# Kernel tuning notes

Measured on AMD Instinct MI355X. Metric: run time of the kernel, lower is better.

The kernel has to match this reference:

```python
import jax, jax.numpy as jnp
import numpy as np

W_KERNEL = 5      # dilation kernel size (w)
K_BG = 0.1        # background weight (k)
RELAX = 5.0       # sigmoid temperature (relax)
INF = 1e4         # 'no zero in column' sentinel (>> image diagonal)
EPS = 1e-7        # DiceLoss eps


def setup_inputs() -> dict:
    key = jax.random.key(0)
    k1, k2 = jax.random.split(key)
    B, H, W = 32, 256, 256
    preds = jax.random.normal(k1, (B, H, W), dtype=jnp.float32)
    targets = (jax.random.uniform(k2, (B, H, W)) > 0.99).astype(jnp.float32)
    return {"preds": preds, "targets": targets}


def _dilate(t, w):
    # cv2.dilate with w x w ones kernel == sliding-window max, SAME padding
    pad = w // 2
    return jax.lax.reduce_window(t, -jnp.inf, jax.lax.max,
                                 (1, w, w), (1, 1, 1),
                                 [(0, 0), (pad, pad), (pad, pad)])


def _vertical_dist(zero_mask):
    # per-column distance (in rows) to nearest zero pixel; [B,H,W] -> [B,H,W]
    B, H, W = zero_mask.shape
    rows = jnp.moveaxis(zero_mask, 1, 0)  # [H,B,W]

    def step(carry, z):
        d = jnp.where(z, 0.0, jnp.minimum(carry + 1.0, INF))
        return d, d

    init = jnp.full((B, W), INF, dtype=jnp.float32)
    _, fwd = jax.lax.scan(step, init, rows)
    _, bwd = jax.lax.scan(step, init, rows[::-1])
    g = jnp.minimum(fwd, bwd[::-1])  # [H,B,W]
    return jnp.moveaxis(g, 0, 1)


def _edt(fat):
    # exact euclidean distance transform (distance to nearest zero pixel),
    # separable two-pass: vertical 1D distance, then horizontal min-plus.
    B, H, W = fat.shape
    g = _vertical_dist(fat == 0)  # [B,H,W]
    col = jnp.arange(W, dtype=jnp.float32)
    off2 = (col[:, None] - col[None, :]) ** 2  # [W_j, W_k]

    def per_img(gi):  # gi: [H,W]
        # d2[i,j] = min_k g[i,k]^2 + (j-k)^2   -> [H,W,W] intermediate
        d2 = jnp.min(gi[:, None, :] ** 2 + off2[None, :, :], axis=-1)
        return jnp.sqrt(d2)

    return jax.lax.map(per_img, g)  # sequential over batch caps memory


def _distance_maps(targets):
    fat = _dilate(targets, W_KERNEL)          # [B,H,W]
    d = _edt(fat)                              # [B,H,W]
    soft = jax.nn.sigmoid(d / RELAX)
    soft = soft - jnp.min(soft, axis=(1, 2), keepdims=True)
    mx = jnp.max(soft, axis=(1, 2), keepdims=True)
    soft = soft / jnp.where(mx > 0, mx, 1.0)
    dm_soft = soft + (1.0 - fat) * K_BG
    has_fg = jnp.max(targets, axis=(1, 2), keepdims=True) > 0
    return jnp.where(has_fg, dm_soft, 1.0 - targets)


def reference(preds, targets):
    p = jax.nn.sigmoid(preds)
    dm = jax.lax.stop_gradient(_distance_maps(targets))  # computed in numpy in torch => constant
    pw = p * dm
    bs = pw.shape[0]
    y_pred = pw.reshape(bs, 1, -1)
    y_true = targets.reshape(bs, 1, -1)
    # smp DiceLoss('binary', from_logits=False): dims=(0,2), smooth=0, eps=1e-7
    inter = jnp.sum(y_pred * y_true, axis=(0, 2))
    card = jnp.sum(y_pred + y_true, axis=(0, 2))
    dice = (2.0 * inter) / jnp.maximum(card, EPS)
    loss = 1.0 - dice
    mask = (jnp.sum(y_true, axis=(0, 2)) > 0).astype(loss.dtype)
    return jnp.mean(loss * mask)
```

## Files before the change

### kernel.cpp

```cpp
#include <hip/hip_runtime.h>
#include <math.h>

#define BB 32
#define HH 256
#define WW 256
#define HW (HH*WW)
#define TOT (BB*HW)
#define K_BG 0.1f
#define RELAX 5.0f
#define EPS_D 1e-7

typedef unsigned long long u64;
typedef unsigned short u16;

__device__ __forceinline__ float sigf(float x) { return 1.0f / (1.0f + expf(-x)); }

__global__ void k_maskdil(const float* __restrict__ tg, u64* __restrict__ dmask) {
    __shared__ u64 nz[20][4];
    __shared__ u64 hd[20][4];
    int blk = blockIdx.x;
    int b = blk >> 4, band = blk & 15;
    int r0 = band * 16;
    int t = threadIdx.x, w = t >> 6;
    const float* img = tg + b * HW;
    for (int rr = 0; rr < 20; ++rr) {
        int rg = r0 + rr - 2;
        float v = (rg >= 0 && rg < HH) ? img[rg * WW + t] : 0.0f;
        u64 bal = __ballot(v != 0.0f);
        if ((t & 63) == 0) nz[rr][w] = bal;
    }
    __syncthreads();
    if (t < 80) {
        int rr = t >> 2, k = t & 3;
        u64 m = nz[rr][k];
        u64 ml = (k > 0) ? nz[rr][k - 1] : 0ULL;
        u64 mr = (k < 3) ? nz[rr][k + 1] : 0ULL;
        hd[rr][k] = m | (m << 1) | (m << 2) | (m >> 1) | (m >> 2)
                  | (ml >> 62) | (ml >> 63) | (mr << 62) | (mr << 63);
    }
    __syncthreads();
    if (t < 64) {
        int rr = t >> 2, k = t & 3;
        u64 o = hd[rr][k] | hd[rr + 1][k] | hd[rr + 2][k] | hd[rr + 3][k] | hd[rr + 4][k];
        dmask[b * 1024 + (r0 + rr) * 4 + k] = o;
    }
}

__global__ __launch_bounds__(256) void k_mega(const float* __restrict__ preds,
                                              const float* __restrict__ tg,
                                              const u64* __restrict__ dmask,
                                              float4* __restrict__ part1,
                                              float4* __restrict__ part2) {
    __shared__ u64 mk[1024];
    __shared__ u16 gS[WW];
    __shared__ float red[8][4];
    int row = blockIdx.x;
    int b = row >> 8, i = row & 255;
    int t = threadIdx.x;

    float p  = preds[row * WW + t];
    float tv = tg[row * WW + t];

    const uint4* src4 = (const uint4*)(dmask + b * 1024);
    uint4* mk4 = (uint4*)mk;
    mk4[t] = src4[t];
    mk4[t + 256] = src4[t + 256];
    __syncthreads();

    int j = t, w = j >> 6;
    u64 bitm = 1ULL << (j & 63);
    int fgbit = (mk[i * 4 + w] & bitm) ? 1 : 0;
    int g0 = 0;
    if (fgbit) {
        int up = 10000;
        for (int k = 1; k <= i; ++k)
            if (!(mk[(i - k) * 4 + w] & bitm)) { up = k; break; }
        int dn = 10000;
        for (int k = 1; k < HH - i; ++k)
            if (!(mk[(i + k) * 4 + w] & bitm)) { dn = k; break; }
        g0 = min(up, dn);
    }
    gS[j] = (u16)g0;
    __syncthreads();

    float gv = (float)g0;
    float best = gv * gv;
    for (int r = 1; r < WW; ++r) {
        float rr = (float)(r * r);
        if (rr >= best) break;
        int jl = j - r, jr = j + r;
        if (jl >= 0) { float v = (float)gS[jl]; best = fminf(best, v * v + rr); }
        if (jr < WW) { float v = (float)gS[jr]; best = fminf(best, v * v + rr); }
    }
    float dv = sqrtf(best);

    float sp = sigf(p);
    float sd = sigf(dv / RELAX);
    float vals[8];
    vals[0] = sp * sd * tv;
    vals[1] = sp * tv;
    vals[2] = sp * sd;
    vals[3] = sp;
    vals[4] = sp * (1.0f - (float)fgbit);
    vals[5] = tv;
    vals[6] = dv;
    vals[7] = dv;
    for (int off = 32; off > 0; off >>= 1) {
        #pragma unroll
        for (int q = 0; q < 6; ++q) vals[q] += __shfl_down(vals[q], off, 64);
        vals[6] = fminf(vals[6], __shfl_down(vals[6], off, 64));
        vals[7] = fmaxf(vals[7], __shfl_down(vals[7], off, 64));
    }
    int wid = t >> 6, lane = t & 63;
    if (lane == 0) {
        #pragma unroll
        for (int q = 0; q < 8; ++q) red[q][wid] = vals[q];
    }
    __syncthreads();
    if (t == 0) {
        float s[8];
        #pragma unroll
        for (int q = 0; q < 6; ++q) s[q] = red[q][0] + red[q][1] + red[q][2] + red[q][3];
        s[6] = fminf(fminf(red[6][0], red[6][1]), fminf(red[6][2], red[6][3]));
        s[7] = fmaxf(fmaxf(red[7][0], red[7][1]), fmaxf(red[7][2], red[7][3]));
        part1[row] = make_float4(s[0], s[1], s[2], s[3]);
        part2[row] = make_float4(s[4], s[5], s[6], s[7]);
    }
}

__global__ void k_img(const float4* __restrict__ part1, const float4* __restrict__ part2,
                      float4* __restrict__ imgout) {
    __shared__ float red[8][4];
    int b = blockIdx.x, t = threadIdx.x;
    float4 p1 = part1[b * HH + t];
    float4 p2 = part2[b * HH + t];
    float vals[8] = {p1.x, p1.y, p1.z, p1.w, p2.x, p2.y, p2.z, p2.w};
    for (int off = 32; off > 0; off >>= 1) {
        #pragma unroll
        for (int q = 0; q < 6; ++q) vals[q] += __shfl_down(vals[q], off, 64);
        vals[6] = fminf(vals[6], __shfl_down(vals[6], off, 64));
        vals[7] = fmaxf(vals[7], __shfl_down(vals[7], off, 64));
    }
    int wid = t >> 6, lane = t & 63;
    if (lane == 0) {
        #pragma unroll
        for (int q = 0; q < 8; ++q) red[q][wid] = vals[q];
    }
    __syncthreads();
    if (t == 0) {
        float A  = red[0][0] + red[0][1] + red[0][2] + red[0][3];
        float Bs = red[1][0] + red[1][1] + red[1][2] + red[1][3];
        float Ap = red[2][0] + red[2][1] + red[2][2] + red[2][3];
        float Bp = red[3][0] + red[3][1] + red[3][2] + red[3][3];
        float Cp = red[4][0] + red[4][1] + red[4][2] + red[4][3];
        float T  = red[5][0] + red[5][1] + red[5][2] + red[5][3];
        float dmn = fminf(fminf(red[6][0], red[6][1]), fminf(red[6][2], red[6][3]));
        float dmx = fmaxf(fmaxf(red[7][0], red[7][1]), fmaxf(red[7][2], red[7][3]));
        float inter, card, any;
        if (dmx > 0.0f) {
            float smin = sigf(dmn / RELAX);
            float smax = sigf(dmx / RELAX);
            float m = smax - smin;
            float denom = (m > 0.0f) ? m : 1.0f;
            inter = (A - smin * Bs) / denom;
            card  = (Ap - smin * Bp) / denom + K_BG * Cp + T;
            any = 1.0f;
        } else {
            inter = 0.0f;
            card = Bp - Bs + T;
            any = 0.0f;
        }
        imgout[b] = make_float4(inter, card, any, 0.0f);
    }
}

__global__ void k_fin(const float4* __restrict__ imgout, float* __restrict__ out) {
    if (threadIdx.x == 0) {
        double I = 0.0, C = 0.0;
        int any = 0;
        for (int b = 0; b < BB; ++b) {
            float4 v = imgout[b];
            I += (double)v.x; C += (double)v.y;
            any |= (v.z > 0.0f);
        }
        double dice = 2.0 * I / fmax(C, (double)EPS_D);
        out[0] = any ? (float)(1.0 - dice) : 0.0f;
    }
}

extern "C" void kernel_launch(void* const* d_in, const int* in_sizes, int n_in,
                              void* d_out, int out_size, void* d_ws, size_t ws_size,
                              hipStream_t stream) {
    const float* preds = (const float*)d_in[0];
    const float* tg    = (const float*)d_in[1];
    float* out = (float*)d_out;

    u64* dmask   = (u64*)d_ws;
    float4* part1 = (float4*)(dmask + BB * 1024);
    float4* part2 = part1 + BB * HH;
    float4* imgout = part2 + BB * HH;

    hipLaunchKernelGGL(k_maskdil, dim3(BB * 16), dim3(WW), 0, stream, tg, dmask);
    hipLaunchKernelGGL(k_mega, dim3(BB * HH), dim3(WW), 0, stream, preds, tg, dmask,
                       part1, part2);
    hipLaunchKernelGGL(k_img, dim3(BB), dim3(HH), 0, stream, part1, part2, imgout);
    hipLaunchKernelGGL(k_fin, dim3(1), dim3(64), 0, stream, imgout, out);
}
```

Before: 103.1 us.

## Fuse per-image and final reductions into main kernel via last-block atomics

Removes the separate per-image reduction and final dice kernels. The last block to finish each image, detected with an atomic counter, does that image's reduction, and the last image block computes the scalar loss. It also stops rereading the float targets in the main kernel: the target value is rebuilt from a bitmask written by the mask kernel. This saves two kernel launches and the 8 MB target reread, at the cost of thread fences and atomics, and relies on the counters being reset by the first kernel on every call.

```diff
diff --git a/kernel.cpp b/kernel.cpp
--- a/kernel.cpp
+++ b/kernel.cpp
@@ -15,13 +15,15 @@
 
 __device__ __forceinline__ float sigf(float x) { return 1.0f / (1.0f + expf(-x)); }
 
-__global__ void k_maskdil(const float* __restrict__ tg, u64* __restrict__ dmask) {
+__global__ void k_maskdil(const float* __restrict__ tg, u64* __restrict__ dmask,
+                          u64* __restrict__ nzmask, int* __restrict__ cnt) {
     __shared__ u64 nz[20][4];
     __shared__ u64 hd[20][4];
     int blk = blockIdx.x;
     int b = blk >> 4, band = blk & 15;
     int r0 = band * 16;
     int t = threadIdx.x, w = t >> 6;
+    if (blk == 0 && t < 33) cnt[t] = 0;
     const float* img = tg + b * HW;
     for (int rr = 0; rr < 20; ++rr) {
         int rg = r0 + rr - 2;
@@ -38,6 +40,10 @@
         hd[rr][k] = m | (m << 1) | (m << 2) | (m >> 1) | (m >> 2)
                   | (ml >> 62) | (ml >> 63) | (mr << 62) | (mr << 63);
     }
+    if (t < 64) {
+        int rr = t >> 2, k = t & 3;
+        nzmask[b * 1024 + (r0 + rr) * 4 + k] = nz[rr + 2][k];
+    }
     __syncthreads();
     if (t < 64) {
         int rr = t >> 2, k = t & 3;
@@ -47,19 +53,22 @@
 }
 
 __global__ __launch_bounds__(256) void k_mega(const float* __restrict__ preds,
-                                              const float* __restrict__ tg,
                                               const u64* __restrict__ dmask,
+                                              const u64* __restrict__ nzmask,
                                               float4* __restrict__ part1,
-                                              float4* __restrict__ part2) {
+                                              float4* __restrict__ part2,
+                                              float4* __restrict__ imgout,
+                                              int* __restrict__ cnt,
+                                              float* __restrict__ out) {
     __shared__ u64 mk[1024];
     __shared__ u16 gS[WW];
     __shared__ float red[8][4];
+    __shared__ int lastA;
     int row = blockIdx.x;
     int b = row >> 8, i = row & 255;
     int t = threadIdx.x;
 
-    float p  = preds[row * WW + t];
-    float tv = tg[row * WW + t];
+    float p = preds[row * WW + t];
 
     const uint4* src4 = (const uint4*)(dmask + b * 1024);
     uint4* mk4 = (uint4*)mk;
@@ -69,6 +78,7 @@
 
     int j = t, w = j >> 6;
     u64 bitm = 1ULL << (j & 63);
+    float tv = (float)((nzmask[b * 1024 + i * 4 + w] >> (j & 63)) & 1ULL);
     int fgbit = (mk[i * 4 + w] & bitm) ? 1 : 0;
     int g0 = 0;
     if (fgbit) {
@@ -125,66 +135,67 @@
         s[7] = fmaxf(fmaxf(red[7][0], red[7][1]), fmaxf(red[7][2], red[7][3]));
         part1[row] = make_float4(s[0], s[1], s[2], s[3]);
         part2[row] = make_float4(s[4], s[5], s[6], s[7]);
-    }
-}
-
-__global__ void k_img(const float4* __restrict__ part1, const float4* __restrict__ part2,
-                      float4* __restrict__ imgout) {
-    __shared__ float red[8][4];
-    int b = blockIdx.x, t = threadIdx.x;
-    float4 p1 = part1[b * HH + t];
-    float4 p2 = part2[b * HH + t];
-    float vals[8] = {p1.x, p1.y, p1.z, p1.w, p2.x, p2.y, p2.z, p2.w};
-    for (int off = 32; off > 0; off >>= 1) {
-        #pragma unroll
-        for (int q = 0; q < 6; ++q) vals[q] += __shfl_down(vals[q], off, 64);
-        vals[6] = fminf(vals[6], __shfl_down(vals[6], off, 64));
-        vals[7] = fmaxf(vals[7], __shfl_down(vals[7], off, 64));
-    }
-    int wid = t >> 6, lane = t & 63;
-    if (lane == 0) {
-        #pragma unroll
-        for (int q = 0; q < 8; ++q) red[q][wid] = vals[q];
-    }
-    __syncthreads();
-    if (t == 0) {
-        float A  = red[0][0] + red[0][1] + red[0][2] + red[0][3];
-        float Bs = red[1][0] + red[1][1] + red[1][2] + red[1][3];
-        float Ap = red[2][0] + red[2][1] + red[2][2] + red[2][3];
-        float Bp = red[3][0] + red[3][1] + red[3][2] + red[3][3];
-        float Cp = red[4][0] + red[4][1] + red[4][2] + red[4][3];
-        float T  = red[5][0] + red[5][1] + red[5][2] + red[5][3];
-        float dmn = fminf(fminf(red[6][0], red[6][1]), fminf(red[6][2], red[6][3]));
-        float dmx = fmaxf(fmaxf(red[7][0], red[7][1]), fmaxf(red[7][2], red[7][3]));
-        float inter, card, any;
-        if (dmx > 0.0f) {
-            float smin = sigf(dmn / RELAX);
-            float smax = sigf(dmx / RELAX);
-            float m = smax - smin;
-            float denom = (m > 0.0f) ? m : 1.0f;
-            inter = (A - smin * Bs) / denom;
-            card  = (Ap - smin * Bp) / denom + K_BG * Cp + T;
-            any = 1.0f;
-        } else {
-            inter = 0.0f;
-            card = Bp - Bs + T;
-            any = 0.0f;
-        }
-        imgout[b] = make_float4(inter, card, any, 0.0f);
-    }
-}
-
-__global__ void k_fin(const float4* __restrict__ imgout, float* __restrict__ out) {
-    if (threadIdx.x == 0) {
-        double I = 0.0, C = 0.0;
-        int any = 0;
-        for (int b = 0; b < BB; ++b) {
-            float4 v = imgout[b];
-            I += (double)v.x; C += (double)v.y;
-            any |= (v.z > 0.0f);
-        }
-        double dice = 2.0 * I / fmax(C, (double)EPS_D);
-        out[0] = any ? (float)(1.0 - dice) : 0.0f;
+        __threadfence();
+        int old = atomicAdd(&cnt[b], 1);
+        lastA = (old == 255);
+    }
+    __syncthreads();
+
+    if (lastA) {
+        float4 p1 = part1[b * HH + t];
+        float4 p2 = part2[b * HH + t];
+        float v2[8] = {p1.x, p1.y, p1.z, p1.w, p2.x, p2.y, p2.z, p2.w};
+        for (int off = 32; off > 0; off >>= 1) {
+            #pragma unroll
+            for (int q = 0; q < 6; ++q) v2[q] += __shfl_down(v2[q], off, 64);
+            v2[6] = fminf(v2[6], __shfl_down(v2[6], off, 64));
+            v2[7] = fmaxf(v2[7], __shfl_down(v2[7], off, 64));
+        }
+        if (lane == 0) {
+            #pragma unroll
+            for (int q = 0; q < 8; ++q) red[q][wid] = v2[q];
+        }
+        __syncthreads();
+        int lastB = 0;
+        if (t == 0) {
+            float A  = red[0][0] + red[0][1] + red[0][2] + red[0][3];
+            float Bs = red[1][0] + red[1][1] + red[1][2] + red[1][3];
+            float Ap = red[2][0] + red[2][1] + red[2][2] + red[2][3];
+            float Bp = red[3][0] + red[3][1] + red[3][2] + red[3][3];
+            float Cp = red[4][0] + red[4][1] + red[4][2] + red[4][3];
+            float T  = red[5][0] + red[5][1] + red[5][2] + red[5][3];
+            float dmn = fminf(fminf(red[6][0], red[6][1]), fminf(red[6][2], red[6][3]));
+            float dmx = fmaxf(fmaxf(red[7][0], red[7][1]), fmaxf(red[7][2], red[7][3]));
+            float inter, card, any;
+            if (dmx > 0.0f) {
+                float smin = sigf(dmn / RELAX);
+                float smax = sigf(dmx / RELAX);
+                float m = smax - smin;
+                float denom = (m > 0.0f) ? m : 1.0f;
+                inter = (A - smin * Bs) / denom;
+                card  = (Ap - smin * Bp) / denom + K_BG * Cp + T;
+                any = 1.0f;
+            } else {
+                inter = 0.0f;
+                card = Bp - Bs + T;
+                any = 0.0f;
+            }
+            imgout[b] = make_float4(inter, card, any, 0.0f);
+            __threadfence();
+            int old2 = atomicAdd(&cnt[32], 1);
+            lastB = (old2 == BB - 1);
+        }
+        if (t == 0 && lastB) {
+            double I = 0.0, C = 0.0;
+            int any = 0;
+            for (int bb = 0; bb < BB; ++bb) {
+                float4 v = imgout[bb];
+                I += (double)v.x; C += (double)v.y;
+                any |= (v.z > 0.0f);
+            }
+            double dice = 2.0 * I / fmax(C, (double)EPS_D);
+            out[0] = any ? (float)(1.0 - dice) : 0.0f;
+        }
     }
 }
 
@@ -195,14 +206,14 @@
     const float* tg    = (const float*)d_in[1];
     float* out = (float*)d_out;
 
-    u64* dmask   = (u64*)d_ws;
-    float4* part1 = (float4*)(dmask + BB * 1024);
+    u64* dmask    = (u64*)d_ws;
+    u64* nzmask   = dmask + BB * 1024;
+    float4* part1 = (float4*)(nzmask + BB * 1024);
     float4* part2 = part1 + BB * HH;
     float4* imgout = part2 + BB * HH;
-
-    hipLaunchKernelGGL(k_maskdil, dim3(BB * 16), dim3(WW), 0, stream, tg, dmask);
-    hipLaunchKernelGGL(k_mega, dim3(BB * HH), dim3(WW), 0, stream, preds, tg, dmask,
-                       part1, part2);
-    hipLaunchKernelGGL(k_img, dim3(BB), dim3(HH), 0, stream, part1, part2, imgout);
-    hipLaunchKernelGGL(k_fin, dim3(1), dim3(64), 0, stream, imgout, out);
+    int* cnt = (int*)(imgout + BB);
+
+    hipLaunchKernelGGL(k_maskdil, dim3(BB * 16), dim3(WW), 0, stream, tg, dmask, nzmask, cnt);
+    hipLaunchKernelGGL(k_mega, dim3(BB * HH), dim3(WW), 0, stream, preds, dmask, nzmask,
+                       part1, part2, imgout, cnt, out);
 }
```

New measurement: 247.0 us. 2.4x slower.

## Use bit-transposed column masks and clz/ffs scans for vertical distances, 4 rows per block

Applied to the files above, without the earlier changes.

The dilated mask is now stored column-major per 64-bit word and bit-transposed in registers with shuffle butterflies, so each thread holds its column as four 64-bit words. The nearest zero above and below is then found with clz/ffs instead of a serial per-row loop. Each block handles 4 rows, which amortises the mask transpose and cuts the block count and partial sums. The target values are read from a packed nonzero bitmask rather than the float tensor. This adds transpose and shuffle work per block and raises per-thread register use.

```diff
diff --git a/kernel.cpp b/kernel.cpp
--- a/kernel.cpp
+++ b/kernel.cpp
@@ -5,7 +5,6 @@
 #define HH 256
 #define WW 256
 #define HW (HH*WW)
-#define TOT (BB*HW)
 #define K_BG 0.1f
 #define RELAX 5.0f
 #define EPS_D 1e-7
@@ -15,7 +14,12 @@
 
 __device__ __forceinline__ float sigf(float x) { return 1.0f / (1.0f + expf(-x)); }
 
-__global__ void k_maskdil(const float* __restrict__ tg, u64* __restrict__ dmask) {
+__device__ __forceinline__ u64 shflx64(u64 x, int s) {
+    return (u64)__shfl_xor((unsigned long long)x, s, 64);
+}
+
+__global__ void k_maskdil(const float* __restrict__ tg, u64* __restrict__ dmaskT,
+                          u64* __restrict__ nzmask) {
     __shared__ u64 nz[20][4];
     __shared__ u64 hd[20][4];
     int blk = blockIdx.x;
@@ -38,124 +42,159 @@
         hd[rr][k] = m | (m << 1) | (m << 2) | (m >> 1) | (m >> 2)
                   | (ml >> 62) | (ml >> 63) | (mr << 62) | (mr << 63);
     }
+    if (t < 64) {
+        int rr = t >> 2, k = t & 3;
+        nzmask[b * 1024 + (r0 + rr) * 4 + k] = nz[rr + 2][k];
+    }
     __syncthreads();
     if (t < 64) {
         int rr = t >> 2, k = t & 3;
         u64 o = hd[rr][k] | hd[rr + 1][k] | hd[rr + 2][k] | hd[rr + 3][k] | hd[rr + 4][k];
-        dmask[b * 1024 + (r0 + rr) * 4 + k] = o;
+        dmaskT[b * 1024 + k * 256 + (r0 + rr)] = o;
     }
 }
 
 __global__ __launch_bounds__(256) void k_mega(const float* __restrict__ preds,
-                                              const float* __restrict__ tg,
-                                              const u64* __restrict__ dmask,
+                                              const u64* __restrict__ dmaskT,
+                                              const u64* __restrict__ nzmask,
                                               float4* __restrict__ part1,
                                               float4* __restrict__ part2) {
-    __shared__ u64 mk[1024];
-    __shared__ u16 gS[WW];
+    __shared__ u64 colT[4 * 256];
+    __shared__ u16 gS[4][WW];
     __shared__ float red[8][4];
-    int row = blockIdx.x;
-    int b = row >> 8, i = row & 255;
-    int t = threadIdx.x;
-
-    float p  = preds[row * WW + t];
-    float tv = tg[row * WW + t];
-
-    const uint4* src4 = (const uint4*)(dmask + b * 1024);
-    uint4* mk4 = (uint4*)mk;
-    mk4[t] = src4[t];
-    mk4[t + 256] = src4[t + 256];
-    __syncthreads();
-
-    int j = t, w = j >> 6;
-    u64 bitm = 1ULL << (j & 63);
-    int fgbit = (mk[i * 4 + w] & bitm) ? 1 : 0;
-    int g0 = 0;
-    if (fgbit) {
-        int up = 10000;
-        for (int k = 1; k <= i; ++k)
-            if (!(mk[(i - k) * 4 + w] & bitm)) { up = k; break; }
-        int dn = 10000;
-        for (int k = 1; k < HH - i; ++k)
-            if (!(mk[(i + k) * 4 + w] & bitm)) { dn = k; break; }
-        g0 = min(up, dn);
-    }
-    gS[j] = (u16)g0;
-    __syncthreads();
-
-    float gv = (float)g0;
-    float best = gv * gv;
-    for (int r = 1; r < WW; ++r) {
-        float rr = (float)(r * r);
-        if (rr >= best) break;
-        int jl = j - r, jr = j + r;
-        if (jl >= 0) { float v = (float)gS[jl]; best = fminf(best, v * v + rr); }
-        if (jr < WW) { float v = (float)gS[jr]; best = fminf(best, v * v + rr); }
-    }
-    float dv = sqrtf(best);
-
-    float sp = sigf(p);
-    float sd = sigf(dv / RELAX);
+    int blk = blockIdx.x;
+    int b = blk >> 6, q = blk & 63;
+    int i0 = q * 4;
+    int tid = threadIdx.x;
+    int lane = tid & 63, wv = tid >> 6;
+    int j = tid;
+
+    float p[4];
+    u64 nzw[4];
+    #pragma unroll
+    for (int rr = 0; rr < 4; ++rr) {
+        p[rr] = preds[(b * HH + i0 + rr) * WW + j];
+        nzw[rr] = nzmask[b * 1024 + (i0 + rr) * 4 + (j >> 6)];
+    }
+
+    const u64* base = dmaskT + b * 1024;
+    const u64 L32 = 0x00000000FFFFFFFFULL, L16 = 0x0000FFFF0000FFFFULL,
+              L8  = 0x00FF00FF00FF00FFULL, L4  = 0x0F0F0F0F0F0F0F0FULL,
+              L2  = 0x3333333333333333ULL, L1  = 0x5555555555555555ULL;
+    #pragma unroll
+    for (int w = 0; w < 4; ++w) {
+        u64 x = base[w * 256 + wv * 64 + lane];
+        u64 pp;
+        pp = shflx64(x, 32); x = (lane & 32) ? ((x & ~L32) | ((pp & ~L32) >> 32)) : ((x & L32) | ((pp & L32) << 32));
+        pp = shflx64(x, 16); x = (lane & 16) ? ((x & ~L16) | ((pp & ~L16) >> 16)) : ((x & L16) | ((pp & L16) << 16));
+        pp = shflx64(x,  8); x = (lane &  8) ? ((x & ~L8 ) | ((pp & ~L8 ) >>  8)) : ((x & L8 ) | ((pp & L8 ) <<  8));
+        pp = shflx64(x,  4); x = (lane &  4) ? ((x & ~L4 ) | ((pp & ~L4 ) >>  4)) : ((x & L4 ) | ((pp & L4 ) <<  4));
+        pp = shflx64(x,  2); x = (lane &  2) ? ((x & ~L2 ) | ((pp & ~L2 ) >>  2)) : ((x & L2 ) | ((pp & L2 ) <<  2));
+        pp = shflx64(x,  1); x = (lane &  1) ? ((x & ~L1 ) | ((pp & ~L1 ) >>  1)) : ((x & L1 ) | ((pp & L1 ) <<  1));
+        colT[wv * 256 + w * 64 + lane] = x;
+    }
+    __syncthreads();
+
+    u64 yw[4];
+    #pragma unroll
+    for (int g = 0; g < 4; ++g) yw[g] = ~colT[g * 256 + j];
+
+    int g0v[4], fgv[4];
+    #pragma unroll
+    for (int rr = 0; rr < 4; ++rr) {
+        int i = i0 + rr;
+        int iw = i >> 6, ib = i & 63;
+        u64 lowm  = (2ULL << ib) - 1ULL;
+        u64 highm = ~((1ULL << ib) - 1ULL);
+        int pu = -1, pd = -1;
+        #pragma unroll
+        for (int w = 0; w < 4; ++w) {
+            u64 m = (w < iw) ? ~0ULL : ((w == iw) ? lowm : 0ULL);
+            u64 z = yw[w] & m;
+            int cand = (w << 6) + 63 - __clzll(z);
+            pu = z ? cand : pu;
+        }
+        #pragma unroll
+        for (int w = 3; w >= 0; --w) {
+            u64 m = (w > iw) ? ~0ULL : ((w == iw) ? highm : 0ULL);
+            u64 z = yw[w] & m;
+            int cand = (w << 6) + (__ffsll((unsigned long long)z) - 1);
+            pd = z ? cand : pd;
+        }
+        int up = (pu >= 0) ? (i - pu) : 10000;
+        int dn = (pd >= 0) ? (pd - i) : 10000;
+        int g0 = min(min(up, dn), 10000);
+        g0v[rr] = g0;
+        fgv[rr] = (int)((~yw[iw] >> ib) & 1ULL);
+        gS[rr][j] = (u16)g0;
+    }
+    __syncthreads();
+
     float vals[8];
-    vals[0] = sp * sd * tv;
-    vals[1] = sp * tv;
-    vals[2] = sp * sd;
-    vals[3] = sp;
-    vals[4] = sp * (1.0f - (float)fgbit);
-    vals[5] = tv;
-    vals[6] = dv;
-    vals[7] = dv;
+    #pragma unroll
+    for (int qq = 0; qq < 6; ++qq) vals[qq] = 0.0f;
+    vals[6] = 1e30f; vals[7] = 0.0f;
+    #pragma unroll
+    for (int rr = 0; rr < 4; ++rr) {
+        float gv = (float)g0v[rr];
+        float best = gv * gv;
+        for (int r = 1; r < WW; ++r) {
+            float rf = (float)(r * r);
+            if (rf >= best) break;
+            int jl = j - r, jr = j + r;
+            if (jl >= 0) { float v = (float)gS[rr][jl]; best = fminf(best, v * v + rf); }
+            if (jr < WW) { float v = (float)gS[rr][jr]; best = fminf(best, v * v + rf); }
+        }
+        float dv = sqrtf(best);
+        float sp = sigf(p[rr]);
+        float sd = sigf(dv / RELAX);
+        float tv = (float)((nzw[rr] >> (j & 63)) & 1ULL);
+        vals[0] += sp * sd * tv;
+        vals[1] += sp * tv;
+        vals[2] += sp * sd;
+        vals[3] += sp;
+        vals[4] += fgv[rr] ? 0.0f : sp;
+        vals[5] += tv;
+        vals[6] = fminf(vals[6], dv);
+        vals[7] = fmaxf(vals[7], dv);
+    }
     for (int off = 32; off > 0; off >>= 1) {
         #pragma unroll
-        for (int q = 0; q < 6; ++q) vals[q] += __shfl_down(vals[q], off, 64);
+        for (int qq = 0; qq < 6; ++qq) vals[qq] += __shfl_down(vals[qq], off, 64);
         vals[6] = fminf(vals[6], __shfl_down(vals[6], off, 64));
         vals[7] = fmaxf(vals[7], __shfl_down(vals[7], off, 64));
     }
-    int wid = t >> 6, lane = t & 63;
     if (lane == 0) {
         #pragma unroll
-        for (int q = 0; q < 8; ++q) red[q][wid] = vals[q];
-    }
-    __syncthreads();
-    if (t == 0) {
+        for (int qq = 0; qq < 8; ++qq) red[qq][wv] = vals[qq];
+    }
+    __syncthreads();
+    if (tid == 0) {
         float s[8];
         #pragma unroll
-        for (int q = 0; q < 6; ++q) s[q] = red[q][0] + red[q][1] + red[q][2] + red[q][3];
+        for (int qq = 0; qq < 6; ++qq) s[qq] = red[qq][0] + red[qq][1] + red[qq][2] + red[qq][3];
         s[6] = fminf(fminf(red[6][0], red[6][1]), fminf(red[6][2], red[6][3]));
         s[7] = fmaxf(fmaxf(red[7][0], red[7][1]), fmaxf(red[7][2], red[7][3]));
-        part1[row] = make_float4(s[0], s[1], s[2], s[3]);
-        part2[row] = make_float4(s[4], s[5], s[6], s[7]);
+        part1[blk] = make_float4(s[0], s[1], s[2], s[3]);
+        part2[blk] = make_float4(s[4], s[5], s[6], s[7]);
     }
 }
 
 __global__ void k_img(const float4* __restrict__ part1, const float4* __restrict__ part2,
                       float4* __restrict__ imgout) {
-    __shared__ float red[8][4];
     int b = blockIdx.x, t = threadIdx.x;
-    float4 p1 = part1[b * HH + t];
-    float4 p2 = part2[b * HH + t];
+    float4 p1 = part1[b * 64 + t];
+    float4 p2 = part2[b * 64 + t];
     float vals[8] = {p1.x, p1.y, p1.z, p1.w, p2.x, p2.y, p2.z, p2.w};
     for (int off = 32; off > 0; off >>= 1) {
         #pragma unroll
-        for (int q = 0; q < 6; ++q) vals[q] += __shfl_down(vals[q], off, 64);
+        for (int qq = 0; qq < 6; ++qq) vals[qq] += __shfl_down(vals[qq], off, 64);
         vals[6] = fminf(vals[6], __shfl_down(vals[6], off, 64));
         vals[7] = fmaxf(vals[7], __shfl_down(vals[7], off, 64));
     }
-    int wid = t >> 6, lane = t & 63;
-    if (lane == 0) {
-        #pragma unroll
-        for (int q = 0; q < 8; ++q) red[q][wid] = vals[q];
-    }
-    __syncthreads();
     if (t == 0) {
-        float A  = red[0][0] + red[0][1] + red[0][2] + red[0][3];
-        float Bs = red[1][0] + red[1][1] + red[1][2] + red[1][3];
-        float Ap = red[2][0] + red[2][1] + red[2][2] + red[2][3];
-        float Bp = red[3][0] + red[3][1] + red[3][2] + red[3][3];
-        float Cp = red[4][0] + red[4][1] + red[4][2] + red[4][3];
-        float T  = red[5][0] + red[5][1] + red[5][2] + red[5][3];
-        float dmn = fminf(fminf(red[6][0], red[6][1]), fminf(red[6][2], red[6][3]));
-        float dmx = fmaxf(fmaxf(red[7][0], red[7][1]), fmaxf(red[7][2], red[7][3]));
+        float A = vals[0], Bs = vals[1], Ap = vals[2], Bp = vals[3];
+        float Cp = vals[4], T = vals[5], dmn = vals[6], dmx = vals[7];
         float inter, card, any;
         if (dmx > 0.0f) {
             float smin = sigf(dmn / RELAX);
@@ -195,14 +234,15 @@
     const float* tg    = (const float*)d_in[1];
     float* out = (float*)d_out;
 
-    u64* dmask   = (u64*)d_ws;
-    float4* part1 = (float4*)(dmask + BB * 1024);
-    float4* part2 = part1 + BB * HH;
-    float4* imgout = part2 + BB * HH;
-
-    hipLaunchKernelGGL(k_maskdil, dim3(BB * 16), dim3(WW), 0, stream, tg, dmask);
-    hipLaunchKernelGGL(k_mega, dim3(BB * HH), dim3(WW), 0, stream, preds, tg, dmask,
+    u64* dmaskT   = (u64*)d_ws;
+    u64* nzmask   = dmaskT + BB * 1024;
+    float4* part1 = (float4*)(nzmask + BB * 1024);
+    float4* part2 = part1 + BB * 64;
+    float4* imgout = part2 + BB * 64;
+
+    hipLaunchKernelGGL(k_maskdil, dim3(BB * 16), dim3(WW), 0, stream, tg, dmaskT, nzmask);
+    hipLaunchKernelGGL(k_mega, dim3(BB * 64), dim3(WW), 0, stream, preds, dmaskT, nzmask,
                        part1, part2);
-    hipLaunchKernelGGL(k_img, dim3(BB), dim3(HH), 0, stream, part1, part2, imgout);
+    hipLaunchKernelGGL(k_img, dim3(BB), dim3(64), 0, stream, part1, part2, imgout);
     hipLaunchKernelGGL(k_fin, dim3(1), dim3(64), 0, stream, imgout, out);
 }
```

Result: faster. 95.81 us (-7.1%).
